# Performance work log

Hardware: AMD Instinct MI355X
Metric: run time of the kernel (lower is better)

The kernel has to match this reference:

```python
import jax, jax.numpy as jnp
import numpy as np

B, IN, OUT = 256, 512, 512


def setup_inputs() -> dict:
    key = jax.random.key(0)
    k0, k1, k2, k3, k4, k5 = jax.random.split(key, 6)
    x_mean = jax.random.normal(k0, (B, IN), jnp.float32)
    x_var = jax.random.normal(k1, (B, IN, IN), jnp.float32)
    # params (original inits A_mean to zeros which gives a degenerate test;
    # use small random values for a meaningful numerical baseline)
    xavier_std = float(np.sqrt(2.0 / (IN + OUT)))
    A_mean = jax.random.normal(k2, (IN, OUT), jnp.float32) * xavier_std
    A_var = jax.random.normal(k3, (IN, OUT), jnp.float32) * xavier_std
    b_mean = jax.random.normal(k4, (OUT,), jnp.float32) * 0.01
    b_var = jax.random.normal(k5, (OUT,), jnp.float32)
    return {"x_mean": x_mean, "x_var": x_var, "A_mean": A_mean,
            "A_var": A_var, "b_mean": b_mean, "b_var": b_var}


def reference(x_mean, x_var, A_mean, A_var, b_mean, b_var):
    # y_mean = x A_mean + b_mean   (F.linear(x, A.t()) == x @ A)
    y_mean = x_mean @ A_mean + b_mean  # [B, OUT]

    # E[x x] diagonal: Var[x]_ii + mean_i^2
    x_var_diag = jnp.diagonal(x_var, axis1=1, axis2=2)  # [B, IN]
    xx_mean = x_var_diag + x_mean * x_mean
    term1_diag = xx_mean @ A_var  # [B, OUT]

    # A^T Cov[x] A, full matrix as in original, then take its diagonal
    xCov_A = jnp.einsum('bij,jo->bio', x_var, A_mean)      # [B, IN, OUT]
    A_xCov_A = jnp.einsum('bio,ip->bop', xCov_A, A_mean)   # [B, OUT, OUT]
    term2_diag = jnp.diagonal(A_xCov_A, axis1=1, axis2=2)  # [B, OUT]

    result_diag = term1_diag + term2_diag + b_var
    y_var = jax.vmap(jnp.diag)(result_diag)  # diag_embed -> [B, OUT, OUT]
    return y_mean, y_var
```

## Files before the change

kernel.cpp:

```cpp
#include <hip/hip_runtime.h>
#include <hip/hip_bf16.h>


typedef __bf16 bf16x8 __attribute__((ext_vector_type(8)));
typedef float f32x4 __attribute__((ext_vector_type(4)));

__device__ inline ushort f2bf(float f) {
    union { float f; unsigned u; } x; x.f = f;
    unsigned u = x.u + 0x7fffu + ((x.u >> 16) & 1u);
    return (ushort)(u >> 16);
}

__device__ inline void gload16(const void* g, void* l) {
    __builtin_amdgcn_global_load_lds(
        (const __attribute__((address_space(1))) void*)g,
        (__attribute__((address_space(3))) void*)l, 16, 0, 0);
}

__global__ void k_prep_at(const float* __restrict__ am, ushort* __restrict__ abt) {
    int C = blockIdx.x * 256 + threadIdx.x;
    int nt = C >> 13;
    int L  = C & 8191;
    int ks = L >> 9;
    int rem = L & 511;
    int s = rem >> 3, c = rem & 7;
    int lc = c ^ (s & 7);
    int h = lc >> 2, g = lc & 3;
    int r = 2 * s + h;
    int o = nt * 128 + r;
    int j0 = ks * 32 + g * 8;
    ushort u[8];
    #pragma unroll
    for (int e = 0; e < 8; ++e) u[e] = f2bf(am[(j0 + e) * 512 + o]);
    *(int4*)(abt + (long)C * 8) = *(int4*)u;
}

__global__ void k_diag(const float* __restrict__ xv, const float* __restrict__ xm,
                       float* __restrict__ xx) {
    int idx = blockIdx.x * 256 + threadIdx.x;
    int b = idx >> 9, i = idx & 511;
    float m = xm[idx];
    xx[idx] = xv[(long)b * 262144 + i * 513] + m * m;
}

__global__ void k_t1(const float* __restrict__ xm, const float* __restrict__ xx,
                     const float* __restrict__ am, const float* __restrict__ av,
                     float* __restrict__ yp, float* __restrict__ tp) {
    __shared__ float S[2][64];
    int t = threadIdx.x;
    int b  = blockIdx.x >> 3;
    int ic = blockIdx.x & 7;
    int i0 = ic * 64;
    if (t < 128) {
        int which = t >> 6, ii = t & 63;
        const float* src = which ? xx : xm;
        S[which][ii] = src[b * 512 + i0 + ii];
    }
    __syncthreads();
    int mat = t >> 7;
    int o4 = t & 127;
    const float* M = mat ? av : am;
    const float* Sv = S[mat];
    f32x4 acc = {0.f, 0.f, 0.f, 0.f};
    #pragma unroll 8
    for (int ii = 0; ii < 64; ++ii) {
        f32x4 a = *(const f32x4*)(M + (long)(i0 + ii) * 512 + o4 * 4);
        float s = Sv[ii];
        acc[0] = fmaf(s, a[0], acc[0]);
        acc[1] = fmaf(s, a[1], acc[1]);
        acc[2] = fmaf(s, a[2], acc[2]);
        acc[3] = fmaf(s, a[3], acc[3]);
    }
    float* dst = (mat ? tp : yp) + ((long)ic * 256 + b) * 512 + o4 * 4;
    *(f32x4*)dst = acc;
}

__global__ __launch_bounds__(256, 2) void k_gemm2(
        const float*  __restrict__ xv,
        const ushort* __restrict__ abt,
        const float*  __restrict__ amean,
        float* __restrict__ p2,
        float* __restrict__ yvar)
{
    __shared__ float  ldsX[4096];
    __shared__ ushort ldsA[4096];
    __shared__ float  red[2][128];

    int t = threadIdx.x;
    int lane = t & 63;
    int wave = t >> 6;
    int wm = wave >> 1, wn = wave & 1;

    int bid = blockIdx.x;
    int swz = (bid & 7) * 512 + (bid >> 3);
    int mtile = swz >> 2;
    int ntile = swz & 3;
    int n0 = ntile * 128;
    long m0 = (long)mtile * 128;
    int msub = mtile & 3;
    int b = mtile >> 2;

    f32x4 acc[4][4];
    #pragma unroll
    for (int a = 0; a < 4; ++a)
        #pragma unroll
        for (int bq = 0; bq < 4; ++bq)
            acc[a][bq] = (f32x4){0.f, 0.f, 0.f, 0.f};

    const float* xs0 = xv + (m0 + wave * 32 + (lane >> 3)) * 512
                       + ((lane & 7) ^ (lane >> 3)) * 4;
    const char* as0 = (const char*)abt + (long)ntile * 131072
                      + wave * 2048 + lane * 16;

    auto stage = [&](int ks) {
        char* xd = (char*)ldsX + wave * 4096;
        const float* sx = xs0 + ks * 32;
        #pragma unroll
        for (int q = 0; q < 4; ++q)
            gload16(sx + q * 8 * 512, xd + q * 1024);
        char* ad = (char*)ldsA + wave * 2048;
        const char* sa = as0 + (long)ks * 8192;
        gload16(sa, ad);
        gload16(sa + 1024, ad + 1024);
    };

    auto compute = [&]() {
        bf16x8 af[4], bfr[4];
        int g = lane >> 4;
        #pragma unroll
        for (int nf = 0; nf < 4; ++nf) {
            int r = wn * 64 + nf * 16 + (lane & 15);
            int s = r >> 1;
            int chunk = (((r & 1) << 2) | g) ^ (s & 7);
            bfr[nf] = *(const bf16x8*)((const char*)ldsA + s * 128 + (chunk << 4));
        }
        #pragma unroll
        for (int mf = 0; mf < 4; ++mf) {
            int r = wm * 64 + mf * 16 + (lane & 15);
            int sw = r & 7;
            const char* bx = (const char*)ldsX + r * 128;
            f32x4 lo = *(const f32x4*)(bx + (((2 * g) ^ sw) << 4));
            f32x4 hi = *(const f32x4*)(bx + (((2 * g + 1) ^ sw) << 4));
            bf16x8 a;
            a[0] = (__bf16)lo[0]; a[1] = (__bf16)lo[1];
            a[2] = (__bf16)lo[2]; a[3] = (__bf16)lo[3];
            a[4] = (__bf16)hi[0]; a[5] = (__bf16)hi[1];
            a[6] = (__bf16)hi[2]; a[7] = (__bf16)hi[3];
            af[mf] = a;
        }
        #pragma unroll
        for (int mf = 0; mf < 4; ++mf)
            #pragma unroll
            for (int nf = 0; nf < 4; ++nf)
                acc[mf][nf] = __builtin_amdgcn_mfma_f32_16x16x32_bf16(
                    af[mf], bfr[nf], acc[mf][nf], 0, 0, 0);
    };

    float* zb = yvar + ((long)b * 512 + msub * 128 + ntile * 32) * 512 + t * 4;
    float4 z = make_float4(0.f, 0.f, 0.f, 0.f);

    for (int ks = 0; ks < 16; ++ks) {
        stage(ks);
        __syncthreads();
        *(float4*)(zb + (long)ks * 1024) = z;
        compute();
        __syncthreads();
    }

    #pragma unroll
    for (int nf = 0; nf < 4; ++nf) {
        float p = 0.f;
        int o = n0 + wn * 64 + nf * 16 + (lane & 15);
        #pragma unroll
        for (int mf = 0; mf < 4; ++mf) {
            #pragma unroll
            for (int j = 0; j < 4; ++j) {
                int i = msub * 128 + wm * 64 + mf * 16 + ((lane >> 4) * 4) + j;
                p += acc[mf][nf][j] * amean[i * 512 + o];
            }
        }
        p += __shfl_xor(p, 16, 64);
        p += __shfl_xor(p, 32, 64);
        if (lane < 16) red[wm][wn * 64 + nf * 16 + lane] = p;
    }
    __syncthreads();
    if (t < 128) {
        float v = red[0][t] + red[1][t];
        p2[((long)b * 4 + msub) * 512 + n0 + t] = v;
    }
}

__global__ void k_final(const float* __restrict__ yp, const float* __restrict__ tp,
                        const float* __restrict__ p2,
                        const float* __restrict__ bm, const float* __restrict__ bv,
                        float* __restrict__ ymean, float* __restrict__ yvar) {
    int idx = blockIdx.x * 256 + threadIdx.x;
    int b = idx >> 9, o = idx & 511;
    float ym = bm[o], t1 = bv[o];
    #pragma unroll
    for (int ic = 0; ic < 8; ++ic) {
        ym += yp[((long)ic * 256 + b) * 512 + o];
        t1 += tp[((long)ic * 256 + b) * 512 + o];
    }
    long pb = (long)b * 2048 + o;
    t1 += p2[pb] + p2[pb + 512] + p2[pb + 1024] + p2[pb + 1536];
    ymean[idx] = ym;
    yvar[(long)idx * 512 + o] = t1;
}

extern "C" void kernel_launch(void* const* d_in, const int* in_sizes, int n_in,
                              void* d_out, int out_size, void* d_ws, size_t ws_size,
                              hipStream_t stream) {
    const float* x_mean = (const float*)d_in[0];
    const float* x_var  = (const float*)d_in[1];
    const float* A_mean = (const float*)d_in[2];
    const float* A_var  = (const float*)d_in[3];
    const float* b_mean = (const float*)d_in[4];
    const float* b_var  = (const float*)d_in[5];

    float* ymean = (float*)d_out;
    float* yvar  = (float*)d_out + 131072;

    char* ws = (char*)d_ws;
    ushort* abt = (ushort*)ws;
    float*  p2  = (float*)(ws + 512 * 1024);
    float*  yp  = (float*)(ws + 2560 * 1024);
    float*  tp  = (float*)(ws + 6656 * 1024);
    float*  xx  = (float*)(ws + 10752 * 1024);

    k_prep_at<<<128, 256, 0, stream>>>(A_mean, abt);
    k_diag<<<512, 256, 0, stream>>>(x_var, x_mean, xx);
    k_t1<<<2048, 256, 0, stream>>>(x_mean, xx, A_mean, A_var, yp, tp);
    k_gemm2<<<4096, 256, 0, stream>>>(x_var, abt, A_mean, p2, yvar);
    k_final<<<512, 256, 0, stream>>>(yp, tp, p2, b_mean, b_var, ymean, yvar);
}
```

Before: 224.3 us.

## Preload full A panel into LDS and stream x_var directly from global

After: 388.7 us. 73.3% more time.

```diff
diff --git a/kernel.cpp b/kernel.cpp
--- a/kernel.cpp
+++ b/kernel.cpp
@@ -19,15 +19,15 @@
 
 __global__ void k_prep_at(const float* __restrict__ am, ushort* __restrict__ abt) {
     int C = blockIdx.x * 256 + threadIdx.x;
-    int nt = C >> 13;
-    int L  = C & 8191;
-    int ks = L >> 9;
-    int rem = L & 511;
+    int nt = C >> 12;
+    int L  = C & 4095;
+    int ks = L >> 8;
+    int rem = L & 255;
     int s = rem >> 3, c = rem & 7;
     int lc = c ^ (s & 7);
     int h = lc >> 2, g = lc & 3;
     int r = 2 * s + h;
-    int o = nt * 128 + r;
+    int o = nt * 64 + r;
     int j0 = ks * 32 + g * 8;
     ushort u[8];
     #pragma unroll
@@ -82,110 +82,94 @@
         float* __restrict__ p2,
         float* __restrict__ yvar)
 {
-    __shared__ float  ldsX[4096];
-    __shared__ ushort ldsA[4096];
-    __shared__ float  red[2][128];
+    __shared__ ushort ldsA[32768];
+    __shared__ float  red[4][64];
 
     int t = threadIdx.x;
     int lane = t & 63;
-    int wave = t >> 6;
-    int wm = wave >> 1, wn = wave & 1;
+    int w = t >> 6;
 
     int bid = blockIdx.x;
-    int swz = (bid & 7) * 512 + (bid >> 3);
-    int mtile = swz >> 2;
-    int ntile = swz & 3;
-    int n0 = ntile * 128;
+    int xcd = bid & 7;
+    int rr  = bid >> 3;
+    int nt  = rr & 7;
+    int mtile = xcd + (rr >> 3) * 8;
     long m0 = (long)mtile * 128;
+    int n0 = nt * 64;
     int msub = mtile & 3;
     int b = mtile >> 2;
 
-    f32x4 acc[4][4];
-    #pragma unroll
-    for (int a = 0; a < 4; ++a)
-        #pragma unroll
-        for (int bq = 0; bq < 4; ++bq)
-            acc[a][bq] = (f32x4){0.f, 0.f, 0.f, 0.f};
-
-    const float* xs0 = xv + (m0 + wave * 32 + (lane >> 3)) * 512
-                       + ((lane & 7) ^ (lane >> 3)) * 4;
-    const char* as0 = (const char*)abt + (long)ntile * 131072
-                      + wave * 2048 + lane * 16;
-
-    auto stage = [&](int ks) {
-        char* xd = (char*)ldsX + wave * 4096;
-        const float* sx = xs0 + ks * 32;
-        #pragma unroll
-        for (int q = 0; q < 4; ++q)
-            gload16(sx + q * 8 * 512, xd + q * 1024);
-        char* ad = (char*)ldsA + wave * 2048;
-        const char* sa = as0 + (long)ks * 8192;
-        gload16(sa, ad);
-        gload16(sa + 1024, ad + 1024);
-    };
-
-    auto compute = [&]() {
-        bf16x8 af[4], bfr[4];
-        int g = lane >> 4;
+    {
+        const char* src = (const char*)abt + (long)nt * 65536 + w * 16384 + lane * 16;
+        char* dst = (char*)ldsA + w * 16384;
+        #pragma unroll
+        for (int q = 0; q < 16; ++q)
+            gload16(src + q * 1024, dst + q * 1024);
+    }
+    __syncthreads();
+
+    f32x4 acc[2][4];
+    #pragma unroll
+    for (int mf = 0; mf < 2; ++mf)
+        #pragma unroll
+        for (int nf = 0; nf < 4; ++nf)
+            acc[mf][nf] = (f32x4){0.f, 0.f, 0.f, 0.f};
+
+    int rl = lane & 15;
+    int g  = lane >> 4;
+    const float* xr0 = xv + (m0 + w * 32 + rl) * 512 + g * 8;
+    float* zb = yvar + ((long)b * 512 + msub * 128 + nt * 16) * 512;
+    float4 z = make_float4(0.f, 0.f, 0.f, 0.f);
+
+    #pragma unroll
+    for (int ks = 0; ks < 16; ++ks) {
+        float4 xa0 = *(const float4*)(xr0 + ks * 32);
+        float4 xa1 = *(const float4*)(xr0 + ks * 32 + 4);
+        float4 xb0 = *(const float4*)(xr0 + 16 * 512 + ks * 32);
+        float4 xb1 = *(const float4*)(xr0 + 16 * 512 + ks * 32 + 4);
+        if (ks < 8)
+            *(float4*)(zb + ((long)ks * 256 + t) * 4) = z;
+        bf16x8 af0, af1;
+        af0[0] = (__bf16)xa0.x; af0[1] = (__bf16)xa0.y;
+        af0[2] = (__bf16)xa0.z; af0[3] = (__bf16)xa0.w;
+        af0[4] = (__bf16)xa1.x; af0[5] = (__bf16)xa1.y;
+        af0[6] = (__bf16)xa1.z; af0[7] = (__bf16)xa1.w;
+        af1[0] = (__bf16)xb0.x; af1[1] = (__bf16)xb0.y;
+        af1[2] = (__bf16)xb0.z; af1[3] = (__bf16)xb0.w;
+        af1[4] = (__bf16)xb1.x; af1[5] = (__bf16)xb1.y;
+        af1[6] = (__bf16)xb1.z; af1[7] = (__bf16)xb1.w;
         #pragma unroll
         for (int nf = 0; nf < 4; ++nf) {
-            int r = wn * 64 + nf * 16 + (lane & 15);
-            int s = r >> 1;
-            int chunk = (((r & 1) << 2) | g) ^ (s & 7);
-            bfr[nf] = *(const bf16x8*)((const char*)ldsA + s * 128 + (chunk << 4));
+            int ro = nf * 16 + rl;
+            int s = ro >> 1, h = ro & 1;
+            bf16x8 bf = *(const bf16x8*)((const char*)ldsA + ks * 4096 + s * 128
+                          + (((((h << 2) | g)) ^ (s & 7)) << 4));
+            acc[0][nf] = __builtin_amdgcn_mfma_f32_16x16x32_bf16(
+                af0, bf, acc[0][nf], 0, 0, 0);
+            acc[1][nf] = __builtin_amdgcn_mfma_f32_16x16x32_bf16(
+                af1, bf, acc[1][nf], 0, 0, 0);
         }
-        #pragma unroll
-        for (int mf = 0; mf < 4; ++mf) {
-            int r = wm * 64 + mf * 16 + (lane & 15);
-            int sw = r & 7;
-            const char* bx = (const char*)ldsX + r * 128;
-            f32x4 lo = *(const f32x4*)(bx + (((2 * g) ^ sw) << 4));
-            f32x4 hi = *(const f32x4*)(bx + (((2 * g + 1) ^ sw) << 4));
-            bf16x8 a;
-            a[0] = (__bf16)lo[0]; a[1] = (__bf16)lo[1];
-            a[2] = (__bf16)lo[2]; a[3] = (__bf16)lo[3];
-            a[4] = (__bf16)hi[0]; a[5] = (__bf16)hi[1];
-            a[6] = (__bf16)hi[2]; a[7] = (__bf16)hi[3];
-            af[mf] = a;
-        }
-        #pragma unroll
-        for (int mf = 0; mf < 4; ++mf)
-            #pragma unroll
-            for (int nf = 0; nf < 4; ++nf)
-                acc[mf][nf] = __builtin_amdgcn_mfma_f32_16x16x32_bf16(
-                    af[mf], bfr[nf], acc[mf][nf], 0, 0, 0);
-    };
-
-    float* zb = yvar + ((long)b * 512 + msub * 128 + ntile * 32) * 512 + t * 4;
-    float4 z = make_float4(0.f, 0.f, 0.f, 0.f);
-
-    for (int ks = 0; ks < 16; ++ks) {
-        stage(ks);
-        __syncthreads();
-        *(float4*)(zb + (long)ks * 1024) = z;
-        compute();
-        __syncthreads();
     }
 
     #pragma unroll
     for (int nf = 0; nf < 4; ++nf) {
         float p = 0.f;
-        int o = n0 + wn * 64 + nf * 16 + (lane & 15);
-        #pragma unroll
-        for (int mf = 0; mf < 4; ++mf) {
+        int o = n0 + nf * 16 + rl;
+        #pragma unroll
+        for (int mf = 0; mf < 2; ++mf) {
             #pragma unroll
             for (int j = 0; j < 4; ++j) {
-                int i = msub * 128 + wm * 64 + mf * 16 + ((lane >> 4) * 4) + j;
+                int i = msub * 128 + w * 32 + mf * 16 + g * 4 + j;
                 p += acc[mf][nf][j] * amean[i * 512 + o];
             }
         }
         p += __shfl_xor(p, 16, 64);
         p += __shfl_xor(p, 32, 64);
-        if (lane < 16) red[wm][wn * 64 + nf * 16 + lane] = p;
+        if (lane < 16) red[w][nf * 16 + lane] = p;
     }
     __syncthreads();
-    if (t < 128) {
-        float v = red[0][t] + red[1][t];
+    if (t < 64) {
+        float v = red[0][t] + red[1][t] + red[2][t] + red[3][t];
         p2[((long)b * 4 + msub) * 512 + n0 + t] = v;
     }
 }
@@ -231,6 +215,6 @@
     k_prep_at<<<128, 256, 0, stream>>>(A_mean, abt);
     k_diag<<<512, 256, 0, stream>>>(x_var, x_mean, xx);
     k_t1<<<2048, 256, 0, stream>>>(x_mean, xx, A_mean, A_var, yp, tp);
-    k_gemm2<<<4096, 256, 0, stream>>>(x_var, abt, A_mean, p2, yvar);
+    k_gemm2<<<8192, 256, 0, stream>>>(x_var, abt, A_mean, p2, yvar);
     k_final<<<512, 256, 0, stream>>>(yp, tp, p2, b_mean, b_var, ymean, yvar);
 }
```
